# Kernel optimization log

Measured on AMD Instinct MI355X. Metric: run time of the kernel, lower is better.

The kernel has to match this reference:

```python
import jax, jax.numpy as jnp
import numpy as np

K = 8
NMS_RADIUS = 5
SCORE_THRESHOLD = 0.05
SIGMA = 5.0


def setup_inputs() -> dict:
    key = jax.random.key(0)
    k1, k2 = jax.random.split(key)
    heatmap = jax.random.normal(k1, (16, 1, 256, 256), dtype=jnp.float32)
    feature_map = jax.random.normal(k2, (16, 128, 256, 256), dtype=jnp.float32)
    return {"heatmap": heatmap, "feature_map": feature_map}


def _extract_topk_peaks(heatmap):
    # heatmap: [B, 1, H, W]
    B, _, H, W = heatmap.shape
    hm = heatmap[:, 0]  # [B, H, W]
    r = NMS_RADIUS
    # max-pool NMS with -inf padding (== torch pad(-inf) + max_pool2d)
    hm_max = jax.lax.reduce_window(
        hm, -jnp.inf, jax.lax.max,
        window_dimensions=(1, 2 * r + 1, 2 * r + 1),
        window_strides=(1, 1, 1),
        padding=((0, 0), (r, r), (r, r)))
    gmax = jnp.max(hm.reshape(B, -1), axis=1).reshape(B, 1, 1)
    is_peak = (hm >= hm_max) & (hm >= gmax * SCORE_THRESHOLD)
    flat_hm = hm.reshape(B, -1)
    flat_peak = is_peak.reshape(B, -1)
    flat_scores = flat_hm * flat_peak.astype(flat_hm.dtype) \
        + (~flat_peak).astype(flat_hm.dtype) * (-1e9)
    topk_scores, topk_idx = jax.lax.top_k(flat_scores, K)  # [B, K]
    rows = topk_idx // W
    cols = topk_idx % W
    positions = jnp.stack([rows.astype(jnp.float32), cols.astype(jnp.float32)], axis=-1)  # [B,K,2]
    probs = jax.nn.softmax(topk_scores, axis=-1)
    valid = topk_scores > -1e8
    return positions, probs, valid


def _bilinear_sample_at_peaks(feature_map, positions):
    # feature_map: [B, C, H, W], positions: [B, K, 2] (row, col) pixel coords
    # torch grid_sample(align_corners=True, zeros pad): coords stay in-bounds,
    # so clipped bilinear interpolation is exact.
    B, C, H, W = feature_map.shape
    fmt = jnp.transpose(feature_map, (0, 2, 3, 1))  # [B, H, W, C]
    rr = positions[..., 0]
    cc = positions[..., 1]
    r0 = jnp.floor(rr)
    c0 = jnp.floor(cc)
    wr = rr - r0  # [B, K]
    wc = cc - c0
    r0i = jnp.clip(r0.astype(jnp.int32), 0, H - 1)
    r1i = jnp.clip(r0.astype(jnp.int32) + 1, 0, H - 1)
    c0i = jnp.clip(c0.astype(jnp.int32), 0, W - 1)
    c1i = jnp.clip(c0.astype(jnp.int32) + 1, 0, W - 1)
    b = jnp.arange(B)[:, None]  # [B, 1]
    f00 = fmt[b, r0i, c0i]  # [B, K, C]
    f01 = fmt[b, r0i, c1i]
    f10 = fmt[b, r1i, c0i]
    f11 = fmt[b, r1i, c1i]
    wr = wr[..., None]
    wc = wc[..., None]
    return (f00 * (1 - wr) * (1 - wc) + f01 * (1 - wr) * wc
            + f10 * wr * (1 - wc) + f11 * wr * wc)  # [B, K, C]


def _reweight_heatmap(heatmap, positions, weights, valid):
    # heatmap: [B,1,H,W]; positions: [B,K,2]; weights/valid: [B,K]
    B, _, H, W = heatmap.shape
    grid_r = jnp.arange(H, dtype=jnp.float32)[:, None]  # [H, 1]
    grid_c = jnp.arange(W, dtype=jnp.float32)[None, :]  # [1, W]
    pr = positions[:, :, 0][:, :, None, None]  # [B, K, 1, 1]
    pc = positions[:, :, 1][:, :, None, None]
    pw = weights[:, :, None, None]
    pv = valid.astype(jnp.float32)[:, :, None, None]
    dist_sq = (grid_r - pr) ** 2 + (grid_c - pc) ** 2  # [B, K, H, W]
    gaussians = jnp.exp(-dist_sq / (2.0 * SIGMA ** 2)) * pw * pv
    weight_map = jnp.sum(gaussians, axis=1, keepdims=True)  # [B, 1, H, W]
    weight_map = weight_map / (jnp.max(weight_map, axis=(-1, -2), keepdims=True) + 1e-8)
    return heatmap * (0.5 + 0.5 * weight_map)


def reference(heatmap, feature_map):
    positions, probs, valid = _extract_topk_peaks(heatmap)
    peak_feats = _bilinear_sample_at_peaks(feature_map, positions)
    reweighted = _reweight_heatmap(heatmap, positions, probs, valid)
    return reweighted, peak_feats, positions, probs, valid
```

## Files before the change

### kernel.cpp

```cpp
#include <hip/hip_runtime.h>
#include <math.h>

#define NB 16
#define HH 256
#define WW 256
#define NC 128
#define KTOP 8
#define RAD 5
#define TCAP 125
#define TILE_ROWS 16
#define HALO 5
#define LROWS (TILE_ROWS + 2*HALO)


__global__ void k_nms(const float* __restrict__ hm,
                      float* __restrict__ gpart, int* __restrict__ tcount,
                      float* __restrict__ tv, int* __restrict__ ti) {
    int b    = blockIdx.x >> 4;
    int tile = blockIdx.x & 15;
    int row0 = tile * TILE_ROWS;
    int tid  = threadIdx.x;

    __shared__ float t[LROWS][WW];
    __shared__ float hx[LROWS][WW];
    __shared__ int   cnt;
    __shared__ float red[256];
    if (tid == 0) cnt = 0;

    const float4* p4 = (const float4*)(hm + (size_t)b * HH * WW);
    float4 nf = make_float4(-INFINITY, -INFINITY, -INFINITY, -INFINITY);
    for (int i = tid; i < LROWS * (WW / 4); i += 256) {
        int lr = i >> 6, c4 = i & 63;
        int gr = row0 - HALO + lr;
        float4 v = (gr >= 0 && gr < HH) ? p4[gr * 64 + c4] : nf;
        ((float4*)&t[lr][0])[c4] = v;
    }
    __syncthreads();

    for (int i = tid; i < LROWS * WW; i += 256) {
        int lr = i >> 8, col = i & 255;
        int c0 = col - RAD < 0 ? 0 : col - RAD;
        int c1 = col + RAD > WW - 1 ? WW - 1 : col + RAD;
        float m = -INFINITY;
        for (int c = c0; c <= c1; ++c) m = fmaxf(m, t[lr][c]);
        hx[lr][col] = m;
    }
    __syncthreads();

    float tmax = -INFINITY;
    int tile_id = b * 16 + tile;
    for (int i = tid; i < TILE_ROWS * WW; i += 256) {
        int lr = (i >> 8) + HALO, col = i & 255;
        float v = t[lr][col];
        tmax = fmaxf(tmax, v);
        float m = -INFINITY;
        for (int r = lr - RAD; r <= lr + RAD; ++r) m = fmaxf(m, hx[r][col]);
        if (v >= m) {
            int pos = atomicAdd(&cnt, 1);
            if (pos < TCAP) {
                tv[tile_id * TCAP + pos] = v;
                ti[tile_id * TCAP + pos] = (row0 + lr - HALO) * WW + col;
            }
        }
    }
    red[tid] = tmax;
    __syncthreads();
    for (int s = 128; s > 0; s >>= 1) {
        if (tid < s) red[tid] = fmaxf(red[tid], red[tid + s]);
        __syncthreads();
    }
    if (tid == 0) {
        gpart[tile_id]  = red[0];
        tcount[tile_id] = cnt;
    }
}

__global__ void k_select(const float* __restrict__ fmap,
                         const float* __restrict__ gpart, const int* __restrict__ tcount,
                         const float* __restrict__ tv, const int* __restrict__ ti,
                         float* __restrict__ out_feats, float* __restrict__ out_pos,
                         float* __restrict__ out_probs, float* __restrict__ out_valid,
                         float* __restrict__ pr, float* __restrict__ pc, float* __restrict__ pw) {
    int b = blockIdx.x, tid = threadIdx.x;

    __shared__ float cv[16 * TCAP];
    __shared__ int   ci[16 * TCAP];
    __shared__ int   cnt;
    __shared__ int   sct[16];
    __shared__ float sg;
    if (tid == 0) {
        cnt = 0;
        float g = -INFINITY;
        for (int j = 0; j < 16; ++j) g = fmaxf(g, gpart[b * 16 + j]);
        sg = g;
    }
    if (tid < 16) {
        int c = tcount[b * 16 + tid];
        sct[tid] = c > TCAP ? TCAP : c;
    }
    __syncthreads();
    float thresh = 0.05f * sg;

    for (int i = tid; i < 16 * TCAP; i += 256) {
        int j = i / TCAP, p = i - j * TCAP;
        if (p < sct[j]) {
            float v = tv[(b * 16 + j) * TCAP + p];
            if (v >= thresh) {
                int pos = atomicAdd(&cnt, 1);
                cv[pos] = v;
                ci[pos] = ti[(b * 16 + j) * TCAP + p];
            }
        }
    }
    __syncthreads();
    int count = cnt;

    __shared__ float wv[4]; __shared__ int wi[4]; __shared__ int wp[4];
    __shared__ float sel_v[KTOP]; __shared__ int sel_i[KTOP]; __shared__ int sel_p[KTOP];

    for (int k = 0; k < KTOP; ++k) {
        float bv = -INFINITY; int bi = 0x7fffffff; int bp = -1;
        for (int i = tid; i < count; i += 256) {
            float v = cv[i]; int idx = ci[i];
            if (v > bv || (v == bv && idx < bi)) { bv = v; bi = idx; bp = i; }
        }
        for (int s = 1; s < 64; s <<= 1) {
            float v = __shfl_xor(bv, s); int idx = __shfl_xor(bi, s); int p = __shfl_xor(bp, s);
            if (v > bv || (v == bv && idx < bi)) { bv = v; bi = idx; bp = p; }
        }
        if ((tid & 63) == 0) { int w = tid >> 6; wv[w] = bv; wi[w] = bi; wp[w] = bp; }
        __syncthreads();
        if (tid == 0) {
            for (int j = 1; j < 4; ++j)
                if (wv[j] > wv[0] || (wv[j] == wv[0] && wi[j] < wi[0])) {
                    wv[0] = wv[j]; wi[0] = wi[j]; wp[0] = wp[j];
                }
            sel_v[k] = wv[0]; sel_i[k] = wi[0]; sel_p[k] = wp[0];
            if (wp[0] >= 0) cv[wp[0]] = -INFINITY;
        }
        __syncthreads();
    }

    __shared__ float s_r[KTOP], s_c[KTOP];
    if (tid == 0) {
        int next = 0;
        for (int k = 0; k < KTOP; ++k) {
            if (sel_p[k] < 0) {
                for (;;) {
                    bool taken = false;
                    for (int j = 0; j < count; ++j) if (ci[j] == next) { taken = true; break; }
                    if (!taken) break;
                    ++next;
                }
                sel_i[k] = next;
                sel_v[k] = -1.0e9f;
                ++next;
            }
        }
        float m = sel_v[0];
        for (int k = 1; k < KTOP; ++k) m = fmaxf(m, sel_v[k]);
        float e[KTOP], s = 0.f;
        for (int k = 0; k < KTOP; ++k) { e[k] = expf(sel_v[k] - m); s += e[k]; }
        for (int k = 0; k < KTOP; ++k) {
            float prob = e[k] / s;
            int idx = sel_i[k];
            float rrow = (float)(idx / WW);
            float rcol = (float)(idx % WW);
            float vld  = sel_v[k] > -1.0e8f ? 1.f : 0.f;
            out_pos[(b * KTOP + k) * 2 + 0] = rrow;
            out_pos[(b * KTOP + k) * 2 + 1] = rcol;
            out_probs[b * KTOP + k] = prob;
            out_valid[b * KTOP + k] = vld;
            pr[b * KTOP + k] = rrow;
            pc[b * KTOP + k] = rcol;
            pw[b * KTOP + k] = prob * vld;
            s_r[k] = rrow; s_c[k] = rcol;
        }
    }
    __syncthreads();

    for (int t = tid; t < KTOP * NC; t += 256) {
        int k  = t >> 7;
        int ch = t & 127;
        float rr = s_r[k], cc = s_c[k];
        float r0f = floorf(rr), c0f = floorf(cc);
        float wr = rr - r0f, wc = cc - c0f;
        int r0 = min(max((int)r0f, 0), HH - 1);
        int r1 = min(max((int)r0f + 1, 0), HH - 1);
        int c0 = min(max((int)c0f, 0), WW - 1);
        int c1 = min(max((int)c0f + 1, 0), WW - 1);
        const float* fb = fmap + ((size_t)b * NC + ch) * HH * WW;
        float f00 = fb[r0 * WW + c0], f01 = fb[r0 * WW + c1];
        float f10 = fb[r1 * WW + c0], f11 = fb[r1 * WW + c1];
        out_feats[(size_t)b * KTOP * NC + t] =
            f00 * (1 - wr) * (1 - wc) + f01 * (1 - wr) * wc +
            f10 * wr * (1 - wc) + f11 * wr * wc;
    }
}

__device__ __forceinline__ float wm_at(int pix, const float* spr, const float* spc, const float* spw) {
    float fi = (float)(pix >> 8);
    float fj = (float)(pix & 255);
    float wmv = 0.f;
#pragma unroll
    for (int k = 0; k < KTOP; ++k) {
        float dr = fi - spr[k];
        float dc = fj - spc[k];
        wmv += spw[k] * __expf(-(dr * dr + dc * dc) * 0.02f);
    }
    return wmv;
}

__global__ void k_wmmax(const float* __restrict__ pr, const float* __restrict__ pc,
                        const float* __restrict__ pw, float* __restrict__ wmpart) {
    int b = blockIdx.y, blk = blockIdx.x, tid = threadIdx.x;
    __shared__ float spr[KTOP], spc[KTOP], spw[KTOP];
    if (tid < KTOP) {
        spr[tid] = pr[b * KTOP + tid];
        spc[tid] = pc[b * KTOP + tid];
        spw[tid] = pw[b * KTOP + tid];
    }
    __syncthreads();
    float m = 0.f;
    int pix0 = blk * 1024;
    for (int u = 0; u < 4; ++u)
        m = fmaxf(m, wm_at(pix0 + u * 256 + tid, spr, spc, spw));
    __shared__ float red[256];
    red[tid] = m;
    __syncthreads();
    for (int s = 128; s > 0; s >>= 1) {
        if (tid < s) red[tid] = fmaxf(red[tid], red[tid + s]);
        __syncthreads();
    }
    if (tid == 0) wmpart[b * 64 + blk] = red[0];
}

__global__ void k_reweight(const float* __restrict__ hm,
                           const float* __restrict__ pr, const float* __restrict__ pc,
                           const float* __restrict__ pw, const float* __restrict__ wmpart,
                           float* __restrict__ out) {
    int b = blockIdx.y, blk = blockIdx.x, tid = threadIdx.x;
    __shared__ float spr[KTOP], spc[KTOP], spw[KTOP];
    __shared__ float red[64];
    if (tid < KTOP) {
        spr[tid] = pr[b * KTOP + tid];
        spc[tid] = pc[b * KTOP + tid];
        spw[tid] = pw[b * KTOP + tid];
    }
    if (tid < 64) red[tid] = wmpart[b * 64 + tid];
    __syncthreads();
    if (tid < 32) red[tid] = fmaxf(red[tid], red[tid + 32]); __syncthreads();
    if (tid < 16) red[tid] = fmaxf(red[tid], red[tid + 16]); __syncthreads();
    if (tid < 8)  red[tid] = fmaxf(red[tid], red[tid + 8]);  __syncthreads();
    if (tid < 4)  red[tid] = fmaxf(red[tid], red[tid + 4]);  __syncthreads();
    if (tid < 2)  red[tid] = fmaxf(red[tid], red[tid + 2]);  __syncthreads();
    if (tid < 1)  red[tid] = fmaxf(red[tid], red[tid + 1]);  __syncthreads();
    float inv = 0.5f / (red[0] + 1e-8f);

    int idx4 = blk * 256 + tid;
    const float4* h4 = (const float4*)(hm + (size_t)b * HH * WW);
    float4*       o4 = (float4*)(out + (size_t)b * HH * WW);
    float4 h = h4[idx4];
    int pix = idx4 * 4;
    float4 o;
    o.x = h.x * (0.5f + wm_at(pix + 0, spr, spc, spw) * inv);
    o.y = h.y * (0.5f + wm_at(pix + 1, spr, spc, spw) * inv);
    o.z = h.z * (0.5f + wm_at(pix + 2, spr, spc, spw) * inv);
    o.w = h.w * (0.5f + wm_at(pix + 3, spr, spc, spw) * inv);
    o4[idx4] = o;
}

extern "C" void kernel_launch(void* const* d_in, const int* in_sizes, int n_in,
                              void* d_out, int out_size, void* d_ws, size_t ws_size,
                              hipStream_t stream) {
    const float* heatmap = (const float*)d_in[0];
    const float* fmap    = (const float*)d_in[1];

    float* out = (float*)d_out;
    float* out_reweighted = out;
    float* out_feats      = out + 1048576;
    float* out_pos        = out + 1048576 + 16384;
    float* out_probs      = out_pos + 256;
    float* out_valid      = out_probs + 128;

    char* ws = (char*)d_ws;
    float* tv     = (float*)(ws + 0);
    int*   ti     = (int*)  (ws + 128000);
    int*   tcount = (int*)  (ws + 256000);
    float* gpart  = (float*)(ws + 257024);
    float* pr     = (float*)(ws + 258048);
    float* pc     = (float*)(ws + 258560);
    float* pw     = (float*)(ws + 259072);
    float* wmpart = (float*)(ws + 259584);

    k_nms<<<NB * 16, 256, 0, stream>>>(heatmap, gpart, tcount, tv, ti);
    k_select<<<NB, 256, 0, stream>>>(fmap, gpart, tcount, tv, ti,
                                     out_feats, out_pos, out_probs, out_valid, pr, pc, pw);
    k_wmmax<<<dim3(64, NB), 256, 0, stream>>>(pr, pc, pw, wmpart);
    k_reweight<<<dim3(64, NB), 256, 0, stream>>>(heatmap, pr, pc, pw, wmpart, out_reweighted);
}
```

Before: 61.57 us.

## Fuse all stages into one cooperative kernel with grid syncs

Replaces the four separate launches (NMS, select, weight-map max, reweight) with a single cooperative kernel of 256 blocks that moves between phases through grid.sync(). The global max of the weight map is now found only over 23x23 windows around each peak instead of over all pixels. Feature sampling uses a direct gather because peak positions are integers. This removes launch overhead and the full-image max pass. In exchange it depends on cooperative-launch support and pays for two grid-wide barriers, and it assumes the windowed max matches the true max.

```diff
diff --git a/kernel.cpp b/kernel.cpp
--- a/kernel.cpp
+++ b/kernel.cpp
@@ -1,5 +1,8 @@
 #include <hip/hip_runtime.h>
+#include <hip/hip_cooperative_groups.h>
 #include <math.h>
+
+namespace cg = cooperative_groups;
 
 #define NB 16
 #define HH 256
@@ -11,279 +14,29 @@
 #define TILE_ROWS 16
 #define HALO 5
 #define LROWS (TILE_ROWS + 2*HALO)
-
-
-__global__ void k_nms(const float* __restrict__ hm,
-                      float* __restrict__ gpart, int* __restrict__ tcount,
-                      float* __restrict__ tv, int* __restrict__ ti) {
-    int b    = blockIdx.x >> 4;
-    int tile = blockIdx.x & 15;
-    int row0 = tile * TILE_ROWS;
-    int tid  = threadIdx.x;
-
-    __shared__ float t[LROWS][WW];
-    __shared__ float hx[LROWS][WW];
-    __shared__ int   cnt;
-    __shared__ float red[256];
-    if (tid == 0) cnt = 0;
-
-    const float4* p4 = (const float4*)(hm + (size_t)b * HH * WW);
-    float4 nf = make_float4(-INFINITY, -INFINITY, -INFINITY, -INFINITY);
-    for (int i = tid; i < LROWS * (WW / 4); i += 256) {
-        int lr = i >> 6, c4 = i & 63;
-        int gr = row0 - HALO + lr;
-        float4 v = (gr >= 0 && gr < HH) ? p4[gr * 64 + c4] : nf;
-        ((float4*)&t[lr][0])[c4] = v;
-    }
-    __syncthreads();
-
-    for (int i = tid; i < LROWS * WW; i += 256) {
-        int lr = i >> 8, col = i & 255;
-        int c0 = col - RAD < 0 ? 0 : col - RAD;
-        int c1 = col + RAD > WW - 1 ? WW - 1 : col + RAD;
-        float m = -INFINITY;
-        for (int c = c0; c <= c1; ++c) m = fmaxf(m, t[lr][c]);
-        hx[lr][col] = m;
-    }
-    __syncthreads();
-
-    float tmax = -INFINITY;
-    int tile_id = b * 16 + tile;
-    for (int i = tid; i < TILE_ROWS * WW; i += 256) {
-        int lr = (i >> 8) + HALO, col = i & 255;
-        float v = t[lr][col];
-        tmax = fmaxf(tmax, v);
-        float m = -INFINITY;
-        for (int r = lr - RAD; r <= lr + RAD; ++r) m = fmaxf(m, hx[r][col]);
-        if (v >= m) {
-            int pos = atomicAdd(&cnt, 1);
-            if (pos < TCAP) {
-                tv[tile_id * TCAP + pos] = v;
-                ti[tile_id * TCAP + pos] = (row0 + lr - HALO) * WW + col;
-            }
-        }
-    }
-    red[tid] = tmax;
-    __syncthreads();
-    for (int s = 128; s > 0; s >>= 1) {
-        if (tid < s) red[tid] = fmaxf(red[tid], red[tid + s]);
-        __syncthreads();
-    }
-    if (tid == 0) {
-        gpart[tile_id]  = red[0];
-        tcount[tile_id] = cnt;
-    }
-}
-
-__global__ void k_select(const float* __restrict__ fmap,
-                         const float* __restrict__ gpart, const int* __restrict__ tcount,
-                         const float* __restrict__ tv, const int* __restrict__ ti,
-                         float* __restrict__ out_feats, float* __restrict__ out_pos,
-                         float* __restrict__ out_probs, float* __restrict__ out_valid,
-                         float* __restrict__ pr, float* __restrict__ pc, float* __restrict__ pw) {
-    int b = blockIdx.x, tid = threadIdx.x;
-
-    __shared__ float cv[16 * TCAP];
-    __shared__ int   ci[16 * TCAP];
-    __shared__ int   cnt;
-    __shared__ int   sct[16];
-    __shared__ float sg;
-    if (tid == 0) {
-        cnt = 0;
-        float g = -INFINITY;
-        for (int j = 0; j < 16; ++j) g = fmaxf(g, gpart[b * 16 + j]);
-        sg = g;
-    }
-    if (tid < 16) {
-        int c = tcount[b * 16 + tid];
-        sct[tid] = c > TCAP ? TCAP : c;
-    }
-    __syncthreads();
-    float thresh = 0.05f * sg;
-
-    for (int i = tid; i < 16 * TCAP; i += 256) {
-        int j = i / TCAP, p = i - j * TCAP;
-        if (p < sct[j]) {
-            float v = tv[(b * 16 + j) * TCAP + p];
-            if (v >= thresh) {
-                int pos = atomicAdd(&cnt, 1);
-                cv[pos] = v;
-                ci[pos] = ti[(b * 16 + j) * TCAP + p];
-            }
-        }
-    }
-    __syncthreads();
-    int count = cnt;
-
-    __shared__ float wv[4]; __shared__ int wi[4]; __shared__ int wp[4];
-    __shared__ float sel_v[KTOP]; __shared__ int sel_i[KTOP]; __shared__ int sel_p[KTOP];
-
-    for (int k = 0; k < KTOP; ++k) {
-        float bv = -INFINITY; int bi = 0x7fffffff; int bp = -1;
-        for (int i = tid; i < count; i += 256) {
-            float v = cv[i]; int idx = ci[i];
-            if (v > bv || (v == bv && idx < bi)) { bv = v; bi = idx; bp = i; }
-        }
-        for (int s = 1; s < 64; s <<= 1) {
-            float v = __shfl_xor(bv, s); int idx = __shfl_xor(bi, s); int p = __shfl_xor(bp, s);
-            if (v > bv || (v == bv && idx < bi)) { bv = v; bi = idx; bp = p; }
-        }
-        if ((tid & 63) == 0) { int w = tid >> 6; wv[w] = bv; wi[w] = bi; wp[w] = bp; }
-        __syncthreads();
-        if (tid == 0) {
-            for (int j = 1; j < 4; ++j)
-                if (wv[j] > wv[0] || (wv[j] == wv[0] && wi[j] < wi[0])) {
-                    wv[0] = wv[j]; wi[0] = wi[j]; wp[0] = wp[j];
-                }
-            sel_v[k] = wv[0]; sel_i[k] = wi[0]; sel_p[k] = wp[0];
-            if (wp[0] >= 0) cv[wp[0]] = -INFINITY;
-        }
-        __syncthreads();
-    }
-
-    __shared__ float s_r[KTOP], s_c[KTOP];
-    if (tid == 0) {
-        int next = 0;
-        for (int k = 0; k < KTOP; ++k) {
-            if (sel_p[k] < 0) {
-                for (;;) {
-                    bool taken = false;
-                    for (int j = 0; j < count; ++j) if (ci[j] == next) { taken = true; break; }
-                    if (!taken) break;
-                    ++next;
-                }
-                sel_i[k] = next;
-                sel_v[k] = -1.0e9f;
-                ++next;
-            }
-        }
-        float m = sel_v[0];
-        for (int k = 1; k < KTOP; ++k) m = fmaxf(m, sel_v[k]);
-        float e[KTOP], s = 0.f;
-        for (int k = 0; k < KTOP; ++k) { e[k] = expf(sel_v[k] - m); s += e[k]; }
-        for (int k = 0; k < KTOP; ++k) {
-            float prob = e[k] / s;
-            int idx = sel_i[k];
-            float rrow = (float)(idx / WW);
-            float rcol = (float)(idx % WW);
-            float vld  = sel_v[k] > -1.0e8f ? 1.f : 0.f;
-            out_pos[(b * KTOP + k) * 2 + 0] = rrow;
-            out_pos[(b * KTOP + k) * 2 + 1] = rcol;
-            out_probs[b * KTOP + k] = prob;
-            out_valid[b * KTOP + k] = vld;
-            pr[b * KTOP + k] = rrow;
-            pc[b * KTOP + k] = rcol;
-            pw[b * KTOP + k] = prob * vld;
-            s_r[k] = rrow; s_c[k] = rcol;
-        }
-    }
-    __syncthreads();
-
-    for (int t = tid; t < KTOP * NC; t += 256) {
-        int k  = t >> 7;
-        int ch = t & 127;
-        float rr = s_r[k], cc = s_c[k];
-        float r0f = floorf(rr), c0f = floorf(cc);
-        float wr = rr - r0f, wc = cc - c0f;
-        int r0 = min(max((int)r0f, 0), HH - 1);
-        int r1 = min(max((int)r0f + 1, 0), HH - 1);
-        int c0 = min(max((int)c0f, 0), WW - 1);
-        int c1 = min(max((int)c0f + 1, 0), WW - 1);
-        const float* fb = fmap + ((size_t)b * NC + ch) * HH * WW;
-        float f00 = fb[r0 * WW + c0], f01 = fb[r0 * WW + c1];
-        float f10 = fb[r1 * WW + c0], f11 = fb[r1 * WW + c1];
-        out_feats[(size_t)b * KTOP * NC + t] =
-            f00 * (1 - wr) * (1 - wc) + f01 * (1 - wr) * wc +
-            f10 * wr * (1 - wc) + f11 * wr * wc;
-    }
-}
-
-__device__ __forceinline__ float wm_at(int pix, const float* spr, const float* spc, const float* spw) {
+#define CMAX 2048
+
+
+struct Phase1Mem { float t[LROWS][WW]; float hx[LROWS][WW]; };
+struct Phase2Mem { float cv[CMAX]; int ci[CMAX]; };
+union SMem { Phase1Mem p1; Phase2Mem p2; };
+
+__device__ __forceinline__ float wm_at(int pix, const float* qr, const float* qc, const float* qw) {
     float fi = (float)(pix >> 8);
     float fj = (float)(pix & 255);
     float wmv = 0.f;
 #pragma unroll
     for (int k = 0; k < KTOP; ++k) {
-        float dr = fi - spr[k];
-        float dc = fj - spc[k];
-        wmv += spw[k] * __expf(-(dr * dr + dc * dc) * 0.02f);
+        float dr = fi - qr[k];
+        float dc = fj - qc[k];
+        wmv += qw[k] * __expf(-(dr * dr + dc * dc) * 0.02f);
     }
     return wmv;
 }
 
-__global__ void k_wmmax(const float* __restrict__ pr, const float* __restrict__ pc,
-                        const float* __restrict__ pw, float* __restrict__ wmpart) {
-    int b = blockIdx.y, blk = blockIdx.x, tid = threadIdx.x;
-    __shared__ float spr[KTOP], spc[KTOP], spw[KTOP];
-    if (tid < KTOP) {
-        spr[tid] = pr[b * KTOP + tid];
-        spc[tid] = pc[b * KTOP + tid];
-        spw[tid] = pw[b * KTOP + tid];
-    }
-    __syncthreads();
-    float m = 0.f;
-    int pix0 = blk * 1024;
-    for (int u = 0; u < 4; ++u)
-        m = fmaxf(m, wm_at(pix0 + u * 256 + tid, spr, spc, spw));
-    __shared__ float red[256];
-    red[tid] = m;
-    __syncthreads();
-    for (int s = 128; s > 0; s >>= 1) {
-        if (tid < s) red[tid] = fmaxf(red[tid], red[tid + s]);
-        __syncthreads();
-    }
-    if (tid == 0) wmpart[b * 64 + blk] = red[0];
-}
-
-__global__ void k_reweight(const float* __restrict__ hm,
-                           const float* __restrict__ pr, const float* __restrict__ pc,
-                           const float* __restrict__ pw, const float* __restrict__ wmpart,
-                           float* __restrict__ out) {
-    int b = blockIdx.y, blk = blockIdx.x, tid = threadIdx.x;
-    __shared__ float spr[KTOP], spc[KTOP], spw[KTOP];
-    __shared__ float red[64];
-    if (tid < KTOP) {
-        spr[tid] = pr[b * KTOP + tid];
-        spc[tid] = pc[b * KTOP + tid];
-        spw[tid] = pw[b * KTOP + tid];
-    }
-    if (tid < 64) red[tid] = wmpart[b * 64 + tid];
-    __syncthreads();
-    if (tid < 32) red[tid] = fmaxf(red[tid], red[tid + 32]); __syncthreads();
-    if (tid < 16) red[tid] = fmaxf(red[tid], red[tid + 16]); __syncthreads();
-    if (tid < 8)  red[tid] = fmaxf(red[tid], red[tid + 8]);  __syncthreads();
-    if (tid < 4)  red[tid] = fmaxf(red[tid], red[tid + 4]);  __syncthreads();
-    if (tid < 2)  red[tid] = fmaxf(red[tid], red[tid + 2]);  __syncthreads();
-    if (tid < 1)  red[tid] = fmaxf(red[tid], red[tid + 1]);  __syncthreads();
-    float inv = 0.5f / (red[0] + 1e-8f);
-
-    int idx4 = blk * 256 + tid;
-    const float4* h4 = (const float4*)(hm + (size_t)b * HH * WW);
-    float4*       o4 = (float4*)(out + (size_t)b * HH * WW);
-    float4 h = h4[idx4];
-    int pix = idx4 * 4;
-    float4 o;
-    o.x = h.x * (0.5f + wm_at(pix + 0, spr, spc, spw) * inv);
-    o.y = h.y * (0.5f + wm_at(pix + 1, spr, spc, spw) * inv);
-    o.z = h.z * (0.5f + wm_at(pix + 2, spr, spc, spw) * inv);
-    o.w = h.w * (0.5f + wm_at(pix + 3, spr, spc, spw) * inv);
-    o4[idx4] = o;
-}
-
-extern "C" void kernel_launch(void* const* d_in, const int* in_sizes, int n_in,
-                              void* d_out, int out_size, void* d_ws, size_t ws_size,
-                              hipStream_t stream) {
-    const float* heatmap = (const float*)d_in[0];
-    const float* fmap    = (const float*)d_in[1];
-
-    float* out = (float*)d_out;
-    float* out_reweighted = out;
-    float* out_feats      = out + 1048576;
-    float* out_pos        = out + 1048576 + 16384;
-    float* out_probs      = out_pos + 256;
-    float* out_valid      = out_probs + 128;
-
-    char* ws = (char*)d_ws;
+__global__ void __launch_bounds__(256, 1)
+fused(const float* __restrict__ hm, const float* __restrict__ fmap,
+      float* __restrict__ out, char* __restrict__ ws) {
     float* tv     = (float*)(ws + 0);
     int*   ti     = (int*)  (ws + 128000);
     int*   tcount = (int*)  (ws + 256000);
@@ -291,11 +44,236 @@
     float* pr     = (float*)(ws + 258048);
     float* pc     = (float*)(ws + 258560);
     float* pw     = (float*)(ws + 259072);
-    float* wmpart = (float*)(ws + 259584);
-
-    k_nms<<<NB * 16, 256, 0, stream>>>(heatmap, gpart, tcount, tv, ti);
-    k_select<<<NB, 256, 0, stream>>>(fmap, gpart, tcount, tv, ti,
-                                     out_feats, out_pos, out_probs, out_valid, pr, pc, pw);
-    k_wmmax<<<dim3(64, NB), 256, 0, stream>>>(pr, pc, pw, wmpart);
-    k_reweight<<<dim3(64, NB), 256, 0, stream>>>(heatmap, pr, pc, pw, wmpart, out_reweighted);
+    float* wmmax  = (float*)(ws + 259584);
+
+    float* out_rw    = out;
+    float* out_feats = out + 1048576;
+    float* out_pos   = out + 1048576 + 16384;
+    float* out_probs = out_pos + 256;
+    float* out_valid = out_probs + 128;
+
+    __shared__ SMem sm;
+    __shared__ float red[256];
+    __shared__ int   redi[256];
+    __shared__ int   cnt;
+    __shared__ int   sct[16];
+    __shared__ float s_r[KTOP], s_c[KTOP], s_w[KTOP];
+    __shared__ float sel_v[KTOP]; __shared__ int sel_i[KTOP]; __shared__ int sel_p[KTOP];
+    __shared__ float qinv;
+
+    int blk = blockIdx.x, tid = threadIdx.x;
+    cg::grid_group grid = cg::this_grid();
+
+    {
+        int b    = blk >> 4;
+        int tile = blk & 15;
+        int row0 = tile * TILE_ROWS;
+        int tile_id = blk;
+        if (tid == 0) cnt = 0;
+
+        const float4* p4 = (const float4*)(hm + (size_t)b * HH * WW);
+        float4 nf = make_float4(-INFINITY, -INFINITY, -INFINITY, -INFINITY);
+        for (int i = tid; i < LROWS * (WW / 4); i += 256) {
+            int lr = i >> 6, c4 = i & 63;
+            int gr = row0 - HALO + lr;
+            float4 v = (gr >= 0 && gr < HH) ? p4[gr * 64 + c4] : nf;
+            ((float4*)&sm.p1.t[lr][0])[c4] = v;
+        }
+        __syncthreads();
+
+        for (int i = tid; i < LROWS * WW; i += 256) {
+            int lr = i >> 8, col = i & 255;
+            int c0 = col - RAD < 0 ? 0 : col - RAD;
+            int c1 = col + RAD > WW - 1 ? WW - 1 : col + RAD;
+            float m = -INFINITY;
+            for (int c = c0; c <= c1; ++c) m = fmaxf(m, sm.p1.t[lr][c]);
+            sm.p1.hx[lr][col] = m;
+        }
+        __syncthreads();
+
+        float tmax = -INFINITY;
+        for (int i = tid; i < TILE_ROWS * WW; i += 256) {
+            int lr = (i >> 8) + HALO, col = i & 255;
+            float v = sm.p1.t[lr][col];
+            tmax = fmaxf(tmax, v);
+            float m = -INFINITY;
+            for (int r = lr - RAD; r <= lr + RAD; ++r) m = fmaxf(m, sm.p1.hx[r][col]);
+            if (v >= m) {
+                int pos = atomicAdd(&cnt, 1);
+                if (pos < TCAP) {
+                    tv[tile_id * TCAP + pos] = v;
+                    ti[tile_id * TCAP + pos] = (row0 + lr - HALO) * WW + col;
+                }
+            }
+        }
+        red[tid] = tmax;
+        __syncthreads();
+        for (int s = 128; s > 0; s >>= 1) {
+            if (tid < s) red[tid] = fmaxf(red[tid], red[tid + s]);
+            __syncthreads();
+        }
+        if (tid == 0) {
+            gpart[tile_id]  = red[0];
+            tcount[tile_id] = cnt > TCAP ? TCAP : cnt;
+        }
+    }
+
+    __threadfence();
+    grid.sync();
+
+    if (blk < NB) {
+        int b = blk;
+        if (tid == 0) {
+            cnt = 0;
+            float g = -INFINITY;
+            for (int j = 0; j < 16; ++j) g = fmaxf(g, gpart[b * 16 + j]);
+            red[0] = 0.05f * g;
+        }
+        if (tid < 16) sct[tid] = tcount[b * 16 + tid];
+        __syncthreads();
+        float thresh = red[0];
+
+        for (int i = tid; i < 16 * TCAP; i += 256) {
+            int j = i / TCAP, p = i - j * TCAP;
+            if (p < sct[j]) {
+                float v = tv[(b * 16 + j) * TCAP + p];
+                if (v >= thresh) {
+                    int pos = atomicAdd(&cnt, 1);
+                    sm.p2.cv[pos] = v;
+                    sm.p2.ci[pos] = ti[(b * 16 + j) * TCAP + p];
+                }
+            }
+        }
+        __syncthreads();
+        int count = cnt;
+
+        for (int k = 0; k < KTOP; ++k) {
+            float bv = -INFINITY; int bi = 0x7fffffff; int bp = -1;
+            for (int i = tid; i < count; i += 256) {
+                float v = sm.p2.cv[i]; int idx = sm.p2.ci[i];
+                if (v > bv || (v == bv && idx < bi)) { bv = v; bi = idx; bp = i; }
+            }
+            for (int s = 1; s < 64; s <<= 1) {
+                float v = __shfl_xor(bv, s); int idx = __shfl_xor(bi, s); int p = __shfl_xor(bp, s);
+                if (v > bv || (v == bv && idx < bi)) { bv = v; bi = idx; bp = p; }
+            }
+            if ((tid & 63) == 0) { int w = tid >> 6; red[w] = bv; redi[w] = bi; redi[64 + w] = bp; }
+            __syncthreads();
+            if (tid == 0) {
+                float v0 = red[0]; int i0 = redi[0]; int p0 = redi[64];
+                for (int j = 1; j < 4; ++j)
+                    if (red[j] > v0 || (red[j] == v0 && redi[j] < i0)) {
+                        v0 = red[j]; i0 = redi[j]; p0 = redi[64 + j];
+                    }
+                sel_v[k] = v0; sel_i[k] = i0; sel_p[k] = p0;
+                if (p0 >= 0) sm.p2.cv[p0] = -INFINITY;
+            }
+            __syncthreads();
+        }
+
+        if (tid == 0) {
+            int next = 0;
+            for (int k = 0; k < KTOP; ++k) {
+                if (sel_p[k] < 0) {
+                    for (;;) {
+                        bool taken = false;
+                        for (int j = 0; j < count; ++j) if (sm.p2.ci[j] == next) { taken = true; break; }
+                        if (!taken) break;
+                        ++next;
+                    }
+                    sel_i[k] = next;
+                    sel_v[k] = -1.0e9f;
+                    ++next;
+                }
+            }
+            float m = sel_v[0];
+            for (int k = 1; k < KTOP; ++k) m = fmaxf(m, sel_v[k]);
+            float e[KTOP], s = 0.f;
+            for (int k = 0; k < KTOP; ++k) { e[k] = expf(sel_v[k] - m); s += e[k]; }
+            for (int k = 0; k < KTOP; ++k) {
+                float prob = e[k] / s;
+                int idx = sel_i[k];
+                float rrow = (float)(idx / WW);
+                float rcol = (float)(idx % WW);
+                float vld  = sel_v[k] > -1.0e8f ? 1.f : 0.f;
+                out_pos[(b * KTOP + k) * 2 + 0] = rrow;
+                out_pos[(b * KTOP + k) * 2 + 1] = rcol;
+                out_probs[b * KTOP + k] = prob;
+                out_valid[b * KTOP + k] = vld;
+                pr[b * KTOP + k] = rrow;
+                pc[b * KTOP + k] = rcol;
+                pw[b * KTOP + k] = prob * vld;
+                s_r[k] = rrow; s_c[k] = rcol; s_w[k] = prob * vld;
+            }
+        }
+        __syncthreads();
+
+        float m = 0.f;
+        for (int i = tid; i < KTOP * 529; i += 256) {
+            int k = i / 529, o = i - k * 529;
+            int rr = (int)s_r[k] + (o / 23) - 11;
+            int cc = (int)s_c[k] + (o % 23) - 11;
+            if (rr >= 0 && rr < HH && cc >= 0 && cc < WW)
+                m = fmaxf(m, wm_at(rr * WW + cc, s_r, s_c, s_w));
+        }
+        red[tid] = m;
+        __syncthreads();
+        for (int s = 128; s > 0; s >>= 1) {
+            if (tid < s) red[tid] = fmaxf(red[tid], red[tid + s]);
+            __syncthreads();
+        }
+        if (tid == 0) wmmax[b] = red[0];
+    }
+
+    __threadfence();
+    grid.sync();
+
+    {
+        int gtid = blk * 256 + tid;
+        if (gtid < NB * KTOP * NC) {
+            int b  = gtid >> 10;
+            int t  = gtid & 1023;
+            int k  = t >> 7, ch = t & 127;
+            int r = (int)pr[b * KTOP + k];
+            int c = (int)pc[b * KTOP + k];
+            out_feats[gtid] = fmap[((size_t)b * NC + ch) * HH * WW + r * WW + c];
+        }
+
+        int b3 = blk >> 4, tile3 = blk & 15;
+        __shared__ float qr[KTOP], qc[KTOP], qw[KTOP];
+        if (tid < KTOP) {
+            qr[tid] = pr[b3 * KTOP + tid];
+            qc[tid] = pc[b3 * KTOP + tid];
+            qw[tid] = pw[b3 * KTOP + tid];
+        }
+        if (tid == 0) qinv = 0.5f / (wmmax[b3] + 1e-8f);
+        __syncthreads();
+        float inv = qinv;
+
+        const float4* h4 = (const float4*)(hm + (size_t)b3 * HH * WW);
+        float4*       o4 = (float4*)(out_rw + (size_t)b3 * HH * WW);
+        for (int u = 0; u < 4; ++u) {
+            int idx4 = tile3 * 1024 + u * 256 + tid;
+            float4 h = h4[idx4];
+            int pix = idx4 * 4;
+            float4 o;
+            o.x = h.x * (0.5f + wm_at(pix + 0, qr, qc, qw) * inv);
+            o.y = h.y * (0.5f + wm_at(pix + 1, qr, qc, qw) * inv);
+            o.z = h.z * (0.5f + wm_at(pix + 2, qr, qc, qw) * inv);
+            o.w = h.w * (0.5f + wm_at(pix + 3, qr, qc, qw) * inv);
+            o4[idx4] = o;
+        }
+    }
 }
+
+extern "C" void kernel_launch(void* const* d_in, const int* in_sizes, int n_in,
+                              void* d_out, int out_size, void* d_ws, size_t ws_size,
+                              hipStream_t stream) {
+    const float* heatmap = (const float*)d_in[0];
+    const float* fmap    = (const float*)d_in[1];
+    float* out = (float*)d_out;
+    char*  ws  = (char*)d_ws;
+
+    void* args[] = { (void*)&heatmap, (void*)&fmap, (void*)&out, (void*)&ws };
+    hipLaunchCooperativeKernel((const void*)fused, dim3(NB * 16), dim3(256), args, 0, stream);
+}
```

After: 145.3 us. 136% more time.

## Fuse weight-map max into select, separable Gaussian reweight, drop bilinear interpolation

Applied to the files above, without the earlier changes.

Removes the k_wmmax kernel. The weight-map maximum is now taken in k_select by evaluating only a 23x23 window around each peak, which is exact here only if the maximum lies inside those windows. k_reweight becomes tile-based and uses a separable Gaussian: it precomputes a per-column exp table and per-row weights in shared memory and replaces per-pixel exps with FMAs. Bilinear sampling becomes a single gather, relying on peak positions being integers. This saves one launch and most of the transcendental work, at the cost of a bounded-window approximation for the max.

```diff
diff --git a/kernel.cpp b/kernel.cpp
--- a/kernel.cpp
+++ b/kernel.cpp
@@ -48,7 +48,7 @@
     __syncthreads();
 
     float tmax = -INFINITY;
-    int tile_id = b * 16 + tile;
+    int tile_id = blockIdx.x;
     for (int i = tid; i < TILE_ROWS * WW; i += 256) {
         int lr = (i >> 8) + HALO, col = i & 255;
         float v = t[lr][col];
@@ -71,8 +71,20 @@
     }
     if (tid == 0) {
         gpart[tile_id]  = red[0];
-        tcount[tile_id] = cnt;
-    }
+        tcount[tile_id] = cnt > TCAP ? TCAP : cnt;
+    }
+}
+
+__device__ __forceinline__ float wm_at_f(float fi, float fj,
+                                         const float* qr, const float* qc, const float* qw) {
+    float wmv = 0.f;
+#pragma unroll
+    for (int k = 0; k < KTOP; ++k) {
+        float dr = fi - qr[k];
+        float dc = fj - qc[k];
+        wmv += qw[k] * __expf(-(dr * dr + dc * dc) * 0.02f);
+    }
+    return wmv;
 }
 
 __global__ void k_select(const float* __restrict__ fmap,
@@ -80,26 +92,28 @@
                          const float* __restrict__ tv, const int* __restrict__ ti,
                          float* __restrict__ out_feats, float* __restrict__ out_pos,
                          float* __restrict__ out_probs, float* __restrict__ out_valid,
-                         float* __restrict__ pr, float* __restrict__ pc, float* __restrict__ pw) {
+                         float* __restrict__ pr, float* __restrict__ pc, float* __restrict__ pw,
+                         float* __restrict__ winv) {
     int b = blockIdx.x, tid = threadIdx.x;
 
     __shared__ float cv[16 * TCAP];
     __shared__ int   ci[16 * TCAP];
     __shared__ int   cnt;
     __shared__ int   sct[16];
-    __shared__ float sg;
+    __shared__ float red[256];
+    __shared__ int   redi[128];
+    __shared__ float sel_v[KTOP]; __shared__ int sel_i[KTOP]; __shared__ int sel_p[KTOP];
+    __shared__ float s_r[KTOP], s_c[KTOP], s_w[KTOP];
+
     if (tid == 0) {
         cnt = 0;
         float g = -INFINITY;
         for (int j = 0; j < 16; ++j) g = fmaxf(g, gpart[b * 16 + j]);
-        sg = g;
-    }
-    if (tid < 16) {
-        int c = tcount[b * 16 + tid];
-        sct[tid] = c > TCAP ? TCAP : c;
-    }
-    __syncthreads();
-    float thresh = 0.05f * sg;
+        red[0] = 0.05f * g;
+    }
+    if (tid < 16) sct[tid] = tcount[b * 16 + tid];
+    __syncthreads();
+    float thresh = red[0];
 
     for (int i = tid; i < 16 * TCAP; i += 256) {
         int j = i / TCAP, p = i - j * TCAP;
@@ -115,9 +129,6 @@
     __syncthreads();
     int count = cnt;
 
-    __shared__ float wv[4]; __shared__ int wi[4]; __shared__ int wp[4];
-    __shared__ float sel_v[KTOP]; __shared__ int sel_i[KTOP]; __shared__ int sel_p[KTOP];
-
     for (int k = 0; k < KTOP; ++k) {
         float bv = -INFINITY; int bi = 0x7fffffff; int bp = -1;
         for (int i = tid; i < count; i += 256) {
@@ -128,20 +139,20 @@
             float v = __shfl_xor(bv, s); int idx = __shfl_xor(bi, s); int p = __shfl_xor(bp, s);
             if (v > bv || (v == bv && idx < bi)) { bv = v; bi = idx; bp = p; }
         }
-        if ((tid & 63) == 0) { int w = tid >> 6; wv[w] = bv; wi[w] = bi; wp[w] = bp; }
+        if ((tid & 63) == 0) { int w = tid >> 6; red[w] = bv; redi[w] = bi; redi[64 + w] = bp; }
         __syncthreads();
         if (tid == 0) {
+            float v0 = red[0]; int i0 = redi[0]; int p0 = redi[64];
             for (int j = 1; j < 4; ++j)
-                if (wv[j] > wv[0] || (wv[j] == wv[0] && wi[j] < wi[0])) {
-                    wv[0] = wv[j]; wi[0] = wi[j]; wp[0] = wp[j];
+                if (red[j] > v0 || (red[j] == v0 && redi[j] < i0)) {
+                    v0 = red[j]; i0 = redi[j]; p0 = redi[64 + j];
                 }
-            sel_v[k] = wv[0]; sel_i[k] = wi[0]; sel_p[k] = wp[0];
-            if (wp[0] >= 0) cv[wp[0]] = -INFINITY;
+            sel_v[k] = v0; sel_i[k] = i0; sel_p[k] = p0;
+            if (p0 >= 0) cv[p0] = -INFINITY;
         }
         __syncthreads();
     }
 
-    __shared__ float s_r[KTOP], s_c[KTOP];
     if (tid == 0) {
         int next = 0;
         for (int k = 0; k < KTOP; ++k) {
@@ -174,100 +185,97 @@
             pr[b * KTOP + k] = rrow;
             pc[b * KTOP + k] = rcol;
             pw[b * KTOP + k] = prob * vld;
-            s_r[k] = rrow; s_c[k] = rcol;
-        }
-    }
-    __syncthreads();
+            s_r[k] = rrow; s_c[k] = rcol; s_w[k] = prob * vld;
+        }
+    }
+    __syncthreads();
+
+    float m = 0.f;
+    for (int i = tid; i < KTOP * 529; i += 256) {
+        int k = i / 529, o = i - k * 529;
+        int rr = (int)s_r[k] + (o / 23) - 11;
+        int cc = (int)s_c[k] + (o % 23) - 11;
+        if (rr >= 0 && rr < HH && cc >= 0 && cc < WW)
+            m = fmaxf(m, wm_at_f((float)rr, (float)cc, s_r, s_c, s_w));
+    }
+    red[tid] = m;
+    __syncthreads();
+    for (int s = 128; s > 0; s >>= 1) {
+        if (tid < s) red[tid] = fmaxf(red[tid], red[tid + s]);
+        __syncthreads();
+    }
+    if (tid == 0) winv[b] = 0.5f / (red[0] + 1e-8f);
 
     for (int t = tid; t < KTOP * NC; t += 256) {
         int k  = t >> 7;
         int ch = t & 127;
-        float rr = s_r[k], cc = s_c[k];
-        float r0f = floorf(rr), c0f = floorf(cc);
-        float wr = rr - r0f, wc = cc - c0f;
-        int r0 = min(max((int)r0f, 0), HH - 1);
-        int r1 = min(max((int)r0f + 1, 0), HH - 1);
-        int c0 = min(max((int)c0f, 0), WW - 1);
-        int c1 = min(max((int)c0f + 1, 0), WW - 1);
-        const float* fb = fmap + ((size_t)b * NC + ch) * HH * WW;
-        float f00 = fb[r0 * WW + c0], f01 = fb[r0 * WW + c1];
-        float f10 = fb[r1 * WW + c0], f11 = fb[r1 * WW + c1];
-        out_feats[(size_t)b * KTOP * NC + t] =
-            f00 * (1 - wr) * (1 - wc) + f01 * (1 - wr) * wc +
-            f10 * wr * (1 - wc) + f11 * wr * wc;
-    }
-}
-
-__device__ __forceinline__ float wm_at(int pix, const float* spr, const float* spc, const float* spw) {
-    float fi = (float)(pix >> 8);
-    float fj = (float)(pix & 255);
-    float wmv = 0.f;
-#pragma unroll
-    for (int k = 0; k < KTOP; ++k) {
-        float dr = fi - spr[k];
-        float dc = fj - spc[k];
-        wmv += spw[k] * __expf(-(dr * dr + dc * dc) * 0.02f);
-    }
-    return wmv;
-}
-
-__global__ void k_wmmax(const float* __restrict__ pr, const float* __restrict__ pc,
-                        const float* __restrict__ pw, float* __restrict__ wmpart) {
-    int b = blockIdx.y, blk = blockIdx.x, tid = threadIdx.x;
-    __shared__ float spr[KTOP], spc[KTOP], spw[KTOP];
-    if (tid < KTOP) {
-        spr[tid] = pr[b * KTOP + tid];
-        spc[tid] = pc[b * KTOP + tid];
-        spw[tid] = pw[b * KTOP + tid];
-    }
-    __syncthreads();
-    float m = 0.f;
-    int pix0 = blk * 1024;
-    for (int u = 0; u < 4; ++u)
-        m = fmaxf(m, wm_at(pix0 + u * 256 + tid, spr, spc, spw));
-    __shared__ float red[256];
-    red[tid] = m;
-    __syncthreads();
-    for (int s = 128; s > 0; s >>= 1) {
-        if (tid < s) red[tid] = fmaxf(red[tid], red[tid + s]);
-        __syncthreads();
-    }
-    if (tid == 0) wmpart[b * 64 + blk] = red[0];
+        int r = (int)s_r[k];
+        int c = (int)s_c[k];
+        out_feats[(size_t)b * KTOP * NC + t] = fmap[((size_t)b * NC + ch) * HH * WW + r * WW + c];
+    }
 }
 
 __global__ void k_reweight(const float* __restrict__ hm,
                            const float* __restrict__ pr, const float* __restrict__ pc,
-                           const float* __restrict__ pw, const float* __restrict__ wmpart,
+                           const float* __restrict__ pw, const float* __restrict__ winv,
                            float* __restrict__ out) {
-    int b = blockIdx.y, blk = blockIdx.x, tid = threadIdx.x;
-    __shared__ float spr[KTOP], spc[KTOP], spw[KTOP];
-    __shared__ float red[64];
+    int tile = blockIdx.x, b = blockIdx.y, tid = threadIdx.x;
+    int row0 = tile * TILE_ROWS;
+
+    __shared__ float fc[KTOP][WW];
+    __shared__ float ar[KTOP][TILE_ROWS];
+    __shared__ float qr[KTOP], qc[KTOP], qw[KTOP];
+    __shared__ float qinv;
+
     if (tid < KTOP) {
-        spr[tid] = pr[b * KTOP + tid];
-        spc[tid] = pc[b * KTOP + tid];
-        spw[tid] = pw[b * KTOP + tid];
-    }
-    if (tid < 64) red[tid] = wmpart[b * 64 + tid];
-    __syncthreads();
-    if (tid < 32) red[tid] = fmaxf(red[tid], red[tid + 32]); __syncthreads();
-    if (tid < 16) red[tid] = fmaxf(red[tid], red[tid + 16]); __syncthreads();
-    if (tid < 8)  red[tid] = fmaxf(red[tid], red[tid + 8]);  __syncthreads();
-    if (tid < 4)  red[tid] = fmaxf(red[tid], red[tid + 4]);  __syncthreads();
-    if (tid < 2)  red[tid] = fmaxf(red[tid], red[tid + 2]);  __syncthreads();
-    if (tid < 1)  red[tid] = fmaxf(red[tid], red[tid + 1]);  __syncthreads();
-    float inv = 0.5f / (red[0] + 1e-8f);
-
-    int idx4 = blk * 256 + tid;
-    const float4* h4 = (const float4*)(hm + (size_t)b * HH * WW);
-    float4*       o4 = (float4*)(out + (size_t)b * HH * WW);
-    float4 h = h4[idx4];
-    int pix = idx4 * 4;
-    float4 o;
-    o.x = h.x * (0.5f + wm_at(pix + 0, spr, spc, spw) * inv);
-    o.y = h.y * (0.5f + wm_at(pix + 1, spr, spc, spw) * inv);
-    o.z = h.z * (0.5f + wm_at(pix + 2, spr, spc, spw) * inv);
-    o.w = h.w * (0.5f + wm_at(pix + 3, spr, spc, spw) * inv);
-    o4[idx4] = o;
+        qr[tid] = pr[b * KTOP + tid];
+        qc[tid] = pc[b * KTOP + tid];
+        qw[tid] = pw[b * KTOP + tid];
+    }
+    if (tid == 0) qinv = winv[b];
+    __syncthreads();
+
+    for (int i = tid; i < KTOP * WW; i += 256) {
+        int k = i >> 8, col = i & 255;
+        float d = (float)col - qc[k];
+        fc[k][col] = __expf(-d * d * 0.02f);
+    }
+    if (tid < KTOP * TILE_ROWS) {
+        int k = tid >> 4, r = tid & 15;
+        float d = (float)(row0 + r) - qr[k];
+        ar[k][r] = qw[k] * __expf(-d * d * 0.02f);
+    }
+    __syncthreads();
+    float inv = qinv;
+
+    int r  = tid >> 4;
+    int cb = (tid & 15) * 4;
+    float a[KTOP];
+#pragma unroll
+    for (int k = 0; k < KTOP; ++k) a[k] = ar[k][r];
+
+    const float4* h4 = (const float4*)(hm + (size_t)b * HH * WW + (size_t)(row0 + r) * WW);
+    float4*       o4 = (float4*)(out + (size_t)b * HH * WW + (size_t)(row0 + r) * WW);
+#pragma unroll
+    for (int u = 0; u < 4; ++u) {
+        int c4 = cb + u;
+        float4 h = h4[c4];
+        float4 w = make_float4(0.f, 0.f, 0.f, 0.f);
+#pragma unroll
+        for (int k = 0; k < KTOP; ++k) {
+            float4 f = ((const float4*)&fc[k][0])[c4];
+            w.x += a[k] * f.x;
+            w.y += a[k] * f.y;
+            w.z += a[k] * f.z;
+            w.w += a[k] * f.w;
+        }
+        float4 o;
+        o.x = h.x * (0.5f + w.x * inv);
+        o.y = h.y * (0.5f + w.y * inv);
+        o.z = h.z * (0.5f + w.z * inv);
+        o.w = h.w * (0.5f + w.w * inv);
+        o4[c4] = o;
+    }
 }
 
 extern "C" void kernel_launch(void* const* d_in, const int* in_sizes, int n_in,
@@ -291,11 +299,11 @@
     float* pr     = (float*)(ws + 258048);
     float* pc     = (float*)(ws + 258560);
     float* pw     = (float*)(ws + 259072);
-    float* wmpart = (float*)(ws + 259584);
+    float* winv   = (float*)(ws + 259584);
 
     k_nms<<<NB * 16, 256, 0, stream>>>(heatmap, gpart, tcount, tv, ti);
     k_select<<<NB, 256, 0, stream>>>(fmap, gpart, tcount, tv, ti,
-                                     out_feats, out_pos, out_probs, out_valid, pr, pc, pw);
-    k_wmmax<<<dim3(64, NB), 256, 0, stream>>>(pr, pc, pw, wmpart);
-    k_reweight<<<dim3(64, NB), 256, 0, stream>>>(heatmap, pr, pc, pw, wmpart, out_reweighted);
-}
+                                     out_feats, out_pos, out_probs, out_valid,
+                                     pr, pc, pw, winv);
+    k_reweight<<<dim3(16, NB), 256, 0, stream>>>(heatmap, pr, pc, pw, winv, out_reweighted);
+}
```

Result: no change. 60.54 us (-1.7%).
